# Kernel optimization log

Measured on AMD Instinct MI355X. Metric: run time of the kernel, lower is better.

The kernel has to match this reference:

```python
import jax, jax.numpy as jnp
import numpy as np

D = 768

def gru_cell(x, h, W_ih, W_hh, b_ih, b_hh):
    # torch.nn.GRUCell math
    gi = x @ W_ih.T + b_ih  # [*, 3D]
    gh = h @ W_hh.T + b_hh
    i_r, i_z, i_n = jnp.split(gi, 3, axis=-1)
    h_r, h_z, h_n = jnp.split(gh, 3, axis=-1)
    r = jax.nn.sigmoid(i_r + h_r)
    z = jax.nn.sigmoid(i_z + h_z)
    n = jnp.tanh(i_n + r * h_n)
    return (1.0 - z) * n + z * h


def setup_inputs() -> dict:
    key = jax.random.key(0)
    ks = jax.random.split(key, 16)
    S, E, N, R = 2048, 32768, 100000, 1000
    w = 0.05  # weight scale to avoid full gate saturation
    return {
        'encoder_output': jax.random.normal(ks[0], (1, D), jnp.float32),
        'sample_mask': jax.random.normal(ks[1], (S, D), jnp.float32),
        'seed_entities': jnp.arange(S, dtype=jnp.int64) if jax.config.jax_enable_x64 else jnp.arange(S, dtype=jnp.int32),
        'edge_heads': jax.random.randint(ks[2], (E,), 0, S),
        'edge_tails': jax.random.randint(ks[3], (E,), 0, N),
        'edge_type': jax.random.randint(ks[4], (E,), 0, R),
        'node2node': jnp.arange(N),
        'old_ndata': jnp.arange(N),
        'relation_embeddings': jax.random.normal(ks[5], (R, D), jnp.float32),
        'W_sub': jax.random.normal(ks[6], (D, D), jnp.float32) * w,
        'b_sub': jax.random.normal(ks[7], (D,), jnp.float32) * w,
        'W_obj': jax.random.normal(ks[8], (D, D), jnp.float32) * w,
        'b_obj': jax.random.normal(ks[9], (D,), jnp.float32) * w,
        'W_ih': jax.random.normal(ks[10], (3 * D, D), jnp.float32) * w,
        'W_hh': jax.random.normal(ks[11], (3 * D, D), jnp.float32) * w,
        'b_ih': jax.random.normal(ks[12], (3 * D,), jnp.float32) * w,
        'b_hh': jax.random.normal(ks[13], (3 * D,), jnp.float32) * w,
        'default_ndata': jax.random.normal(ks[14], (N, D), jnp.float32),  # stands in for torch.randn(768) fill
    }


def reference(encoder_output, sample_mask, seed_entities, edge_heads, edge_tails,
              edge_type, node2node, old_ndata, relation_embeddings,
              W_sub, b_sub, W_obj, b_obj, W_ih, W_hh, b_ih, b_hh, default_ndata):
    S = seed_entities.shape[0]
    E = edge_heads.shape[0]
    N = old_ndata.shape[0]

    # per-seed: sub_embedding = tanh(Linear(sample_mask[i])); r0 = GRUCell(encoder_output, sub)
    sub = jnp.tanh(sample_mask @ W_sub.T + b_sub)                    # [S, D]
    x0 = jnp.broadcast_to(encoder_output, sub.shape)                 # [S, D]
    r0 = gru_cell(x0, sub, W_ih, W_hh, b_ih, b_hh)                   # [S, D]

    # map node id -> seed position (for write-order timestamps)
    seed_pos_of_node = jnp.full((N,), -1, jnp.int32).at[seed_entities].set(
        jnp.arange(S, dtype=jnp.int32))
    edge_seed_pos = seed_pos_of_node[edge_heads]                     # [E]

    # per-edge: rj = GRUCell(r0[head], rel_emb); obj = tanh(Linear(rj))
    rel = relation_embeddings[edge_type]                             # [E, D]
    rj = gru_cell(r0[edge_heads], rel, W_ih, W_hh, b_ih, b_hh)       # [E, D]
    obj = jnp.tanh(rj @ W_obj.T + b_obj)                             # [E, D]

    # writes happen in order seed0, seed0-edges, seed1, seed1-edges, ...
    stride = jnp.int32(E + 1)
    seed_t = jnp.arange(S, dtype=jnp.int32) * stride                 # seed write times
    edge_t = edge_seed_pos * stride + 1 + jnp.arange(E, dtype=jnp.int32)

    best = jnp.full((N,), -1, jnp.int32)
    best = best.at[seed_entities].max(seed_t)
    best = best.at[edge_tails].max(edge_t)

    win_s = best[seed_entities] == seed_t
    win_e = best[edge_tails] == edge_t

    table = jnp.zeros((N, sub.shape[-1]), sub.dtype)
    table = table.at[jnp.where(win_s, seed_entities, N)].set(sub, mode='drop')
    table = table.at[jnp.where(win_e, edge_tails, N)].set(obj, mode='drop')

    ids = node2node[old_ndata]                                       # reindexed node ids
    written = best[ids] >= 0
    return jnp.where(written[:, None], table[ids], default_ndata)    # [N, D]
```

## Files before the change

kernel.cpp:

```cpp
#include <hip/hip_runtime.h>

#define D 768
#define D3 2304

typedef __bf16 bf16x8 __attribute__((ext_vector_type(8)));
typedef float f32x4 __attribute__((ext_vector_type(4)));

__device__ __forceinline__ float b2f(unsigned short u) {
    unsigned int i = ((unsigned int)u) << 16;
    return __builtin_bit_cast(float, i);
}
__device__ __forceinline__ unsigned short f2b(float f) {
    unsigned int i = __builtin_bit_cast(unsigned int, f);
    i += 0x7FFFu + ((i >> 16) & 1u);
    return (unsigned short)(i >> 16);
}
__device__ __forceinline__ float sigm(float x) { return 1.0f / (1.0f + __expf(-x)); }

typedef __attribute__((address_space(1))) const unsigned int* as1p;
typedef __attribute__((address_space(3))) unsigned int* as3p;
__device__ __forceinline__ void glds16(const unsigned short* g, unsigned short* l)
{
    __builtin_amdgcn_global_load_lds((as1p)g, (as3p)l, 16, 0, 0);
}

__global__ void k_cast(const float* __restrict__ in, unsigned short* __restrict__ out, int n)
{
    int i4 = (blockIdx.x * blockDim.x + threadIdx.x) * 4;
    if (i4 >= n) return;
    float4 v = *(const float4*)(in + i4);
    ushort4 u;
    u.x = f2b(v.x); u.y = f2b(v.y); u.z = f2b(v.z); u.w = f2b(v.w);
    *(ushort4*)(out + i4) = u;
}

template<int ACT, bool OBF>
__global__ __launch_bounds__(256)
void gemm_nt128(const unsigned short* __restrict__ A,
                const unsigned short* __restrict__ B,
                const float* __restrict__ bias,
                void* __restrict__ Cv,
                int M, const int* __restrict__ Mptr,
                int N, int K)
{
    if (Mptr) M = *Mptr;
    const int bm = blockIdx.y * 128;
    if (bm >= M) return;
    const int bn = blockIdx.x * 128;
    constexpr int BK = 32;

    __shared__ __align__(16) unsigned short As[128 * BK];
    __shared__ __align__(16) unsigned short Bs[128 * BK];

    const int tid  = threadIdx.x;
    const int wave = tid >> 6;
    const int lane = tid & 63;
    const int wr = wave >> 1, wc = wave & 1;

    const int c0 = wave * 2;
    const int sr = lane >> 2;
    const int sc = (lane & 3) << 3;

    int ra0 = bm + c0 * 16 + sr;         if (ra0 >= M) ra0 = M - 1;
    int ra1 = bm + (c0 + 1) * 16 + sr;   if (ra1 >= M) ra1 = M - 1;
    int rb0 = bn + c0 * 16 + sr;         if (rb0 >= N) rb0 = N - 1;
    int rb1 = bn + (c0 + 1) * 16 + sr;   if (rb1 >= N) rb1 = N - 1;

    const unsigned short* Ag0 = A + (size_t)ra0 * K + sc;
    const unsigned short* Ag1 = A + (size_t)ra1 * K + sc;
    const unsigned short* Bg0 = B + (size_t)rb0 * K + sc;
    const unsigned short* Bg1 = B + (size_t)rb1 * K + sc;
    unsigned short* Al0 = &As[c0 * 512];
    unsigned short* Al1 = &As[(c0 + 1) * 512];
    unsigned short* Bl0 = &Bs[c0 * 512];
    unsigned short* Bl1 = &Bs[(c0 + 1) * 512];

    const int fr = lane & 15;
    const int fk = (lane >> 4) << 3;
    const unsigned short* AsF = &As[(wr * 64 + fr) * BK + fk];
    const unsigned short* BsF = &Bs[(wc * 64 + fr) * BK + fk];

    f32x4 acc[4][4];
#pragma unroll
    for (int m = 0; m < 4; ++m)
#pragma unroll
        for (int n = 0; n < 4; ++n) acc[m][n] = (f32x4)0.0f;

    for (int k0 = 0; k0 < K; k0 += BK) {
        glds16(Ag0 + k0, Al0);
        glds16(Ag1 + k0, Al1);
        glds16(Bg0 + k0, Bl0);
        glds16(Bg1 + k0, Bl1);
        __syncthreads();
        bf16x8 a[4], b[4];
#pragma unroll
        for (int m = 0; m < 4; ++m) a[m] = *(const bf16x8*)(AsF + m * 16 * BK);
#pragma unroll
        for (int n = 0; n < 4; ++n) b[n] = *(const bf16x8*)(BsF + n * 16 * BK);
#pragma unroll
        for (int m = 0; m < 4; ++m)
#pragma unroll
            for (int n = 0; n < 4; ++n)
                acc[m][n] = __builtin_amdgcn_mfma_f32_16x16x32_bf16(a[m], b[n], acc[m][n], 0, 0, 0);
        __syncthreads();
    }

    const int rr = (lane >> 4) << 2;
    const int cc = lane & 15;
#pragma unroll
    for (int m = 0; m < 4; ++m) {
        const int row = bm + wr * 64 + m * 16 + rr;
#pragma unroll
        for (int n = 0; n < 4; ++n) {
            const int col = bn + wc * 64 + n * 16 + cc;
            if (col >= N) continue;
            const float bv = bias ? bias[col] : 0.0f;
#pragma unroll
            for (int r = 0; r < 4; ++r) {
                if (row + r < M) {
                    float v = acc[m][n][r] + bv;
                    if (ACT == 1) v = tanhf(v);
                    if (OBF) ((unsigned short*)Cv)[(size_t)(row + r) * N + col] = f2b(v);
                    else     ((float*)Cv)[(size_t)(row + r) * N + col] = v;
                }
            }
        }
    }
}

__global__ void k_gi0(const float* __restrict__ enc,
                      const float* __restrict__ Wih,
                      const float* __restrict__ bih,
                      float* __restrict__ gi0)
{
    int j = blockIdx.x * 4 + (threadIdx.x >> 6);
    int lane = threadIdx.x & 63;
    if (j >= D3) return;
    const float* w = Wih + (size_t)j * D;
    float s = 0.0f;
    for (int k = lane; k < D; k += 64) s += enc[k] * w[k];
#pragma unroll
    for (int off = 32; off > 0; off >>= 1) s += __shfl_xor(s, off, 64);
    if (lane == 0) gi0[j] = s + bih[j];
}

__global__ void k_r0(const float* __restrict__ gi0, const float* __restrict__ gh,
                     const unsigned short* __restrict__ sub,
                     unsigned short* __restrict__ r0, int S)
{
    int idx = blockIdx.x * blockDim.x + threadIdx.x;
    if (idx >= S * D) return;
    int s = idx / D, d = idx - s * D;
    const float* g = gh + (size_t)s * D3;
    float r = sigm(gi0[d] + g[d]);
    float z = sigm(gi0[D + d] + g[D + d]);
    float n = tanhf(gi0[2 * D + d] + r * g[2 * D + d]);
    float h = b2f(sub[idx]);
    r0[idx] = f2b((1.0f - z) * n + z * h);
}

__global__ void k_seed_st(const int* __restrict__ se, int* __restrict__ seed_pos,
                          int* __restrict__ best, int S, int stride)
{
    int s = blockIdx.x * blockDim.x + threadIdx.x;
    if (s >= S) return;
    int node = se[s];
    atomicMax(&seed_pos[node], s);
    atomicMax(&best[node], s * stride);
}

__global__ void k_edge_time(const int* __restrict__ heads, const int* __restrict__ tails,
                            const int* __restrict__ seed_pos, int* __restrict__ best,
                            int E, int stride)
{
    int e = blockIdx.x * blockDim.x + threadIdx.x;
    if (e >= E) return;
    int p = seed_pos[heads[e]];
    int t = p * stride + 1 + e;
    if (t < 0) return;
    atomicMax(&best[tails[e]], t);
}

__global__ void k_seed_win(const int* __restrict__ se, const int* __restrict__ best,
                           int* __restrict__ winner, int S, int stride)
{
    int s = blockIdx.x * blockDim.x + threadIdx.x;
    if (s >= S) return;
    int node = se[s];
    if (best[node] == s * stride) winner[node] = s;
}

__global__ void k_edge_win(const int* __restrict__ heads, const int* __restrict__ tails,
                           const int* __restrict__ seed_pos, const int* __restrict__ best,
                           int* __restrict__ winner, int E, int S, int stride)
{
    int e = blockIdx.x * blockDim.x + threadIdx.x;
    if (e >= E) return;
    int p = seed_pos[heads[e]];
    int t = p * stride + 1 + e;
    if (t < 0) return;
    int node = tails[e];
    if (best[node] == t) winner[node] = S + e;
}

__global__ void k_compact(const int* __restrict__ best, const int* __restrict__ winner,
                          int* __restrict__ cnt, int* __restrict__ wedge,
                          int* __restrict__ objrow, int N, int S)
{
    int n = blockIdx.x * blockDim.x + threadIdx.x;
    if (n >= N) return;
    int w = winner[n];
    if (best[n] >= 0 && w >= S) {
        int r = atomicAdd(cnt, 1);
        wedge[r] = w - S;
        objrow[n] = r;
    }
}

__global__ void k_edge2(const int* __restrict__ wedge, const int* __restrict__ cntp,
                        const int* __restrict__ heads, const int* __restrict__ types,
                        const float* __restrict__ Gi, const float* __restrict__ Ghr,
                        const float* __restrict__ rel,
                        unsigned short* __restrict__ rjw)
{
    const int W = *cntp;
    const int wave = threadIdx.x >> 6;
    const int lane = threadIdx.x & 63;
    for (int row = blockIdx.x * 4 + wave; row < W; row += gridDim.x * 4) {
        int e = wedge[row];
        int hd = heads[e], t = types[e];
        const float* gi = Gi + (size_t)hd * D3;
        const float* gh = Ghr + (size_t)t * D3;
        const float* rl = rel + (size_t)t * D;
        unsigned short* out = rjw + (size_t)row * D;
#pragma unroll
        for (int i = 0; i < 3; ++i) {
            int d = i * 256 + lane * 4;
            float4 vr = *(const float4*)(gi + d);
            float4 hr = *(const float4*)(gh + d);
            float4 vz = *(const float4*)(gi + D + d);
            float4 hz = *(const float4*)(gh + D + d);
            float4 vn = *(const float4*)(gi + 2 * D + d);
            float4 hn = *(const float4*)(gh + 2 * D + d);
            float4 hh = *(const float4*)(rl + d);
            ushort4 o;
            { float r = sigm(vr.x + hr.x), z = sigm(vz.x + hz.x);
              float n = tanhf(vn.x + r * hn.x);
              o.x = f2b((1.0f - z) * n + z * hh.x); }
            { float r = sigm(vr.y + hr.y), z = sigm(vz.y + hz.y);
              float n = tanhf(vn.y + r * hn.y);
              o.y = f2b((1.0f - z) * n + z * hh.y); }
            { float r = sigm(vr.z + hr.z), z = sigm(vz.z + hz.z);
              float n = tanhf(vn.z + r * hn.z);
              o.z = f2b((1.0f - z) * n + z * hh.z); }
            { float r = sigm(vr.w + hr.w), z = sigm(vz.w + hz.w);
              float n = tanhf(vn.w + r * hn.w);
              o.w = f2b((1.0f - z) * n + z * hh.w); }
            *(ushort4*)(out + d) = o;
        }
    }
}

__global__ void k_out(const int* __restrict__ n2n, const int* __restrict__ oldnd,
                      const int* __restrict__ best, const int* __restrict__ winner,
                      const int* __restrict__ objrow,
                      const unsigned short* __restrict__ sub,
                      const unsigned short* __restrict__ obj,
                      const float* __restrict__ defnd,
                      float* __restrict__ out, int N, int S)
{
    int idx = blockIdx.x * blockDim.x + threadIdx.x;
    const int JP = D / 4;
    if (idx >= N * JP) return;
    int i = idx / JP, j = idx - i * JP;
    int id = n2n[oldnd[i]];
    float4 v;
    if (best[id] >= 0) {
        int w = winner[id];
        const unsigned short* src = (w < S) ? sub + (size_t)w * D + j * 4
                                            : obj + (size_t)objrow[id] * D + j * 4;
        ushort4 u = *(const ushort4*)src;
        v.x = b2f(u.x); v.y = b2f(u.y); v.z = b2f(u.z); v.w = b2f(u.w);
    } else {
        v = *(const float4*)(defnd + (size_t)i * D + j * 4);
    }
    *(float4*)(out + (size_t)i * D + j * 4) = v;
}

extern "C" void kernel_launch(void* const* d_in, const int* in_sizes, int n_in,
                              void* d_out, int out_size, void* d_ws, size_t ws_size,
                              hipStream_t stream)
{
    const float* enc    = (const float*)d_in[0];
    const float* smask  = (const float*)d_in[1];
    const int* seed_ent = (const int*)d_in[2];
    const int* eheads   = (const int*)d_in[3];
    const int* etails   = (const int*)d_in[4];
    const int* etype    = (const int*)d_in[5];
    const int* n2n      = (const int*)d_in[6];
    const int* oldnd    = (const int*)d_in[7];
    const float* rel    = (const float*)d_in[8];
    const float* Wsub   = (const float*)d_in[9];
    const float* bsub   = (const float*)d_in[10];
    const float* Wobj   = (const float*)d_in[11];
    const float* bobj   = (const float*)d_in[12];
    const float* Wih    = (const float*)d_in[13];
    const float* Whh    = (const float*)d_in[14];
    const float* bih    = (const float*)d_in[15];
    const float* bhh    = (const float*)d_in[16];
    const float* defnd  = (const float*)d_in[17];

    const int S = in_sizes[2];
    const int E = in_sizes[3];
    const int N = in_sizes[6];
    const int R = in_sizes[8] / D;
    const int stride = E + 1;
    const int maxW = (E < N) ? E : N;

    char* p = (char*)d_ws;
    auto carve = [&](size_t bytes) -> char* {
        char* r = p; p += (bytes + 255) & ~(size_t)255; return r;
    };
    unsigned short* smask_b = (unsigned short*)carve((size_t)S * D * 2);
    unsigned short* Wsub_b  = (unsigned short*)carve((size_t)D * D * 2);
    unsigned short* Wobj_b  = (unsigned short*)carve((size_t)D * D * 2);
    unsigned short* Wih_b   = (unsigned short*)carve((size_t)D3 * D * 2);
    unsigned short* Whh_b   = (unsigned short*)carve((size_t)D3 * D * 2);
    unsigned short* rel_b   = (unsigned short*)carve((size_t)R * D * 2);
    unsigned short* sub     = (unsigned short*)carve((size_t)S * D * 2);
    unsigned short* r0      = (unsigned short*)carve((size_t)S * D * 2);
    unsigned short* rj      = (unsigned short*)carve((size_t)maxW * D * 2);
    unsigned short* obj     = (unsigned short*)carve((size_t)maxW * D * 2);
    float* gi0 = (float*)carve((size_t)D3 * 4);
    float* gh  = (float*)carve((size_t)S * D3 * 4);
    float* ghr = (float*)carve((size_t)R * D3 * 4);
    int* seed_pos = (int*)carve((size_t)N * 4);
    int* best     = (int*)carve((size_t)N * 4);
    int* winner   = (int*)carve((size_t)N * 4);
    int* wedge    = (int*)carve((size_t)maxW * 4);
    int* objrow   = (int*)carve((size_t)N * 4);
    int* cnt      = (int*)carve(256);

    dim3 blk(256);
    auto g1 = [](int n) { return dim3((n + 255) / 256); };
    auto gemmg = [](int M, int N_) { return dim3(N_ / 128, (M + 127) / 128); };

    hipMemsetAsync(seed_pos, 0xFF, (size_t)N * 4, stream);
    hipMemsetAsync(best,     0xFF, (size_t)N * 4, stream);
    hipMemsetAsync(winner,   0xFF, (size_t)N * 4, stream);
    hipMemsetAsync(cnt,      0x00, 4, stream);

    k_seed_st  <<<g1(S), blk, 0, stream>>>(seed_ent, seed_pos, best, S, stride);
    k_edge_time<<<g1(E), blk, 0, stream>>>(eheads, etails, seed_pos, best, E, stride);
    k_seed_win <<<g1(S), blk, 0, stream>>>(seed_ent, best, winner, S, stride);
    k_edge_win <<<g1(E), blk, 0, stream>>>(eheads, etails, seed_pos, best, winner, E, S, stride);
    k_compact  <<<g1(N), blk, 0, stream>>>(best, winner, cnt, wedge, objrow, N, S);

    k_cast<<<g1(S * D / 4),  blk, 0, stream>>>(smask, smask_b, S * D);
    k_cast<<<g1(D * D / 4),  blk, 0, stream>>>(Wsub,  Wsub_b,  D * D);
    k_cast<<<g1(D * D / 4),  blk, 0, stream>>>(Wobj,  Wobj_b,  D * D);
    k_cast<<<g1(D3 * D / 4), blk, 0, stream>>>(Wih,   Wih_b,   D3 * D);
    k_cast<<<g1(D3 * D / 4), blk, 0, stream>>>(Whh,   Whh_b,   D3 * D);
    k_cast<<<g1(R * D / 4),  blk, 0, stream>>>(rel,   rel_b,   R * D);

    gemm_nt128<1, true><<<gemmg(S, D), blk, 0, stream>>>(
        smask_b, Wsub_b, bsub, sub, S, nullptr, D, D);
    k_gi0<<<dim3((D3 + 3) / 4), blk, 0, stream>>>(enc, Wih, bih, gi0);
    gemm_nt128<0, false><<<gemmg(S, D3), blk, 0, stream>>>(
        sub, Whh_b, bhh, gh, S, nullptr, D3, D);
    k_r0<<<g1(S * D), blk, 0, stream>>>(gi0, gh, sub, r0, S);
    gemm_nt128<0, false><<<gemmg(S, D3), blk, 0, stream>>>(
        r0, Wih_b, bih, gh, S, nullptr, D3, D);
    gemm_nt128<0, false><<<gemmg(R, D3), blk, 0, stream>>>(
        rel_b, Whh_b, bhh, ghr, R, nullptr, D3, D);

    k_edge2<<<dim3(2048), blk, 0, stream>>>(wedge, cnt, eheads, etype, gh, ghr, rel, rj);
    gemm_nt128<1, true><<<gemmg(maxW, D), blk, 0, stream>>>(
        rj, Wobj_b, bobj, obj, maxW, cnt, D, D);

    k_out<<<g1(N * (D / 4)), blk, 0, stream>>>(
        n2n, oldnd, best, winner, objrow, sub, obj, defnd, (float*)d_out, N, S);
}
```

Before: 909.9 us.

## Merge casts and group winning edges by relation type via histogram scan

Six fp32-to-bf16 cast launches become one, and the four memsets become two. The seed and edge winner kernels are merged. The node-wide compaction is replaced by a per-relation-type histogram, a single-block prefix scan and a scatter, so winning edges are stored contiguously by type. The intent is fewer launches, no N-wide compaction pass, and better locality for the ghr and rel gathers in k_edge2. The cost is an extra serial scan kernel and atomics on the histogram.

```diff
diff --git a/kernel.cpp b/kernel.cpp
--- a/kernel.cpp
+++ b/kernel.cpp
@@ -24,14 +24,28 @@
     __builtin_amdgcn_global_load_lds((as1p)g, (as3p)l, 16, 0, 0);
 }
 
-__global__ void k_cast(const float* __restrict__ in, unsigned short* __restrict__ out, int n)
-{
-    int i4 = (blockIdx.x * blockDim.x + threadIdx.x) * 4;
-    if (i4 >= n) return;
-    float4 v = *(const float4*)(in + i4);
+__global__ void k_cast6(const float* __restrict__ s0, const float* __restrict__ s1,
+                        const float* __restrict__ s2, const float* __restrict__ s3,
+                        const float* __restrict__ s4, const float* __restrict__ s5,
+                        unsigned short* __restrict__ d0, unsigned short* __restrict__ d1,
+                        unsigned short* __restrict__ d2, unsigned short* __restrict__ d3,
+                        unsigned short* __restrict__ d4, unsigned short* __restrict__ d5,
+                        int c0, int c1, int c2, int c3, int c4, int c5)
+{
+    int g = blockIdx.x * blockDim.x + threadIdx.x;
+    const float* src; unsigned short* dst; int base;
+    if      (g < c0) { src = s0; dst = d0; base = 0;  }
+    else if (g < c1) { src = s1; dst = d1; base = c0; }
+    else if (g < c2) { src = s2; dst = d2; base = c1; }
+    else if (g < c3) { src = s3; dst = d3; base = c2; }
+    else if (g < c4) { src = s4; dst = d4; base = c3; }
+    else if (g < c5) { src = s5; dst = d5; base = c4; }
+    else return;
+    int i4 = (g - base) * 4;
+    float4 v = *(const float4*)(src + i4);
     ushort4 u;
     u.x = f2b(v.x); u.y = f2b(v.y); u.z = f2b(v.z); u.w = f2b(v.w);
-    *(ushort4*)(out + i4) = u;
+    *(ushort4*)(dst + i4) = u;
 }
 
 template<int ACT, bool OBF>
@@ -181,18 +195,76 @@
     atomicMax(&best[tails[e]], t);
 }
 
-__global__ void k_seed_win(const int* __restrict__ se, const int* __restrict__ best,
-                           int* __restrict__ winner, int S, int stride)
-{
-    int s = blockIdx.x * blockDim.x + threadIdx.x;
-    if (s >= S) return;
-    int node = se[s];
-    if (best[node] == s * stride) winner[node] = s;
-}
-
-__global__ void k_edge_win(const int* __restrict__ heads, const int* __restrict__ tails,
-                           const int* __restrict__ seed_pos, const int* __restrict__ best,
-                           int* __restrict__ winner, int E, int S, int stride)
+__global__ void k_win(const int* __restrict__ se,
+                      const int* __restrict__ heads, const int* __restrict__ tails,
+                      const int* __restrict__ types,
+                      const int* __restrict__ seed_pos, const int* __restrict__ best,
+                      int* __restrict__ winner, int* __restrict__ thist,
+                      int S, int E, int stride)
+{
+    int idx = blockIdx.x * blockDim.x + threadIdx.x;
+    if (idx < S) {
+        int node = se[idx];
+        if (best[node] == idx * stride) winner[node] = idx;
+    } else {
+        int e = idx - S;
+        if (e >= E) return;
+        int p = seed_pos[heads[e]];
+        int t = p * stride + 1 + e;
+        if (t < 0) return;
+        if (best[tails[e]] == t) atomicAdd(&thist[types[e]], 1);
+    }
+}
+
+__global__ void k_scan(const int* __restrict__ thist, int* __restrict__ toff,
+                       int* __restrict__ cnt, int R)
+{
+    __shared__ int wsum[4];
+    __shared__ int chunkbase;
+    const int tid  = threadIdx.x;
+    const int lane = tid & 63;
+    const int wave = tid >> 6;
+    if (tid == 0) chunkbase = 0;
+    __syncthreads();
+    for (int base0 = 0; base0 < R; base0 += 1024) {
+        int v[4]; int s = 0;
+        int base = base0 + tid * 4;
+#pragma unroll
+        for (int j = 0; j < 4; ++j) {
+            int i = base + j;
+            v[j] = (i < R) ? thist[i] : 0;
+            s += v[j];
+        }
+        int tsum = s;
+#pragma unroll
+        for (int off = 1; off < 64; off <<= 1) {
+            int o = __shfl_up(tsum, off, 64);
+            if (lane >= off) tsum += o;
+        }
+        if (lane == 63) wsum[wave] = tsum;
+        __syncthreads();
+        int wbase = 0;
+        for (int w = 0; w < 4; ++w) if (w < wave) wbase += wsum[w];
+        int run = chunkbase + wbase + (tsum - s);
+#pragma unroll
+        for (int j = 0; j < 4; ++j) {
+            int i = base + j;
+            if (i < R) toff[i] = run;
+            run += v[j];
+        }
+        __syncthreads();
+        if (tid == 0) chunkbase += wsum[0] + wsum[1] + wsum[2] + wsum[3];
+        __syncthreads();
+    }
+    if (tid == 0) *cnt = chunkbase;
+}
+
+__global__ void k_scatter(const int* __restrict__ heads, const int* __restrict__ tails,
+                          const int* __restrict__ types,
+                          const int* __restrict__ seed_pos, const int* __restrict__ best,
+                          const int* __restrict__ toff, int* __restrict__ tcur,
+                          int* __restrict__ wedge, int* __restrict__ objrow,
+                          int E, int stride)
 {
     int e = blockIdx.x * blockDim.x + threadIdx.x;
     if (e >= E) return;
@@ -200,21 +272,11 @@
     int t = p * stride + 1 + e;
     if (t < 0) return;
     int node = tails[e];
-    if (best[node] == t) winner[node] = S + e;
-}
-
-__global__ void k_compact(const int* __restrict__ best, const int* __restrict__ winner,
-                          int* __restrict__ cnt, int* __restrict__ wedge,
-                          int* __restrict__ objrow, int N, int S)
-{
-    int n = blockIdx.x * blockDim.x + threadIdx.x;
-    if (n >= N) return;
-    int w = winner[n];
-    if (best[n] >= 0 && w >= S) {
-        int r = atomicAdd(cnt, 1);
-        wedge[r] = w - S;
-        objrow[n] = r;
-    }
+    if (best[node] != t) return;
+    int ty = types[e];
+    int r = toff[ty] + atomicAdd(&tcur[ty], 1);
+    wedge[r] = e;
+    objrow[node] = r;
 }
 
 __global__ void k_edge2(const int* __restrict__ wedge, const int* __restrict__ cntp,
@@ -276,9 +338,9 @@
     int id = n2n[oldnd[i]];
     float4 v;
     if (best[id] >= 0) {
-        int w = winner[id];
-        const unsigned short* src = (w < S) ? sub + (size_t)w * D + j * 4
-                                            : obj + (size_t)objrow[id] * D + j * 4;
+        int orow = objrow[id];
+        const unsigned short* src = (orow >= 0) ? obj + (size_t)orow * D + j * 4
+                                                : sub + (size_t)winner[id] * D + j * 4;
         ushort4 u = *(const ushort4*)src;
         v.x = b2f(u.x); v.y = b2f(u.y); v.z = b2f(u.z); v.w = b2f(u.w);
     } else {
@@ -334,34 +396,42 @@
     float* gi0 = (float*)carve((size_t)D3 * 4);
     float* gh  = (float*)carve((size_t)S * D3 * 4);
     float* ghr = (float*)carve((size_t)R * D3 * 4);
-    int* seed_pos = (int*)carve((size_t)N * 4);
-    int* best     = (int*)carve((size_t)N * 4);
-    int* winner   = (int*)carve((size_t)N * 4);
-    int* wedge    = (int*)carve((size_t)maxW * 4);
-    int* objrow   = (int*)carve((size_t)N * 4);
-    int* cnt      = (int*)carve(256);
+    int* ints4    = (int*)carve((size_t)4 * N * 4);
+    int* seed_pos = ints4;
+    int* best     = ints4 + N;
+    int* winner   = ints4 + 2 * (size_t)N;
+    int* objrow   = ints4 + 3 * (size_t)N;
+    int* zblk  = (int*)carve(((size_t)3 * R + 64) * 4);
+    int* thist = zblk;
+    int* tcur  = zblk + R;
+    int* toff  = zblk + 2 * (size_t)R;
+    int* cnt   = zblk + 3 * (size_t)R;
+    int* wedge = (int*)carve((size_t)maxW * 4);
 
     dim3 blk(256);
     auto g1 = [](int n) { return dim3((n + 255) / 256); };
     auto gemmg = [](int M, int N_) { return dim3(N_ / 128, (M + 127) / 128); };
 
-    hipMemsetAsync(seed_pos, 0xFF, (size_t)N * 4, stream);
-    hipMemsetAsync(best,     0xFF, (size_t)N * 4, stream);
-    hipMemsetAsync(winner,   0xFF, (size_t)N * 4, stream);
-    hipMemsetAsync(cnt,      0x00, 4, stream);
+    hipMemsetAsync(ints4, 0xFF, (size_t)4 * N * 4, stream);
+    hipMemsetAsync(zblk,  0x00, ((size_t)3 * R + 64) * 4, stream);
+
+    const int gc0 = S * D / 4;
+    const int gc1 = gc0 + D * D / 4;
+    const int gc2 = gc1 + D * D / 4;
+    const int gc3 = gc2 + D3 * D / 4;
+    const int gc4 = gc3 + D3 * D / 4;
+    const int gc5 = gc4 + R * D / 4;
+    k_cast6<<<g1(gc5), blk, 0, stream>>>(smask, Wsub, Wobj, Wih, Whh, rel,
+                                         smask_b, Wsub_b, Wobj_b, Wih_b, Whh_b, rel_b,
+                                         gc0, gc1, gc2, gc3, gc4, gc5);
 
     k_seed_st  <<<g1(S), blk, 0, stream>>>(seed_ent, seed_pos, best, S, stride);
     k_edge_time<<<g1(E), blk, 0, stream>>>(eheads, etails, seed_pos, best, E, stride);
-    k_seed_win <<<g1(S), blk, 0, stream>>>(seed_ent, best, winner, S, stride);
-    k_edge_win <<<g1(E), blk, 0, stream>>>(eheads, etails, seed_pos, best, winner, E, S, stride);
-    k_compact  <<<g1(N), blk, 0, stream>>>(best, winner, cnt, wedge, objrow, N, S);
-
-    k_cast<<<g1(S * D / 4),  blk, 0, stream>>>(smask, smask_b, S * D);
-    k_cast<<<g1(D * D / 4),  blk, 0, stream>>>(Wsub,  Wsub_b,  D * D);
-    k_cast<<<g1(D * D / 4),  blk, 0, stream>>>(Wobj,  Wobj_b,  D * D);
-    k_cast<<<g1(D3 * D / 4), blk, 0, stream>>>(Wih,   Wih_b,   D3 * D);
-    k_cast<<<g1(D3 * D / 4), blk, 0, stream>>>(Whh,   Whh_b,   D3 * D);
-    k_cast<<<g1(R * D / 4),  blk, 0, stream>>>(rel,   rel_b,   R * D);
+    k_win      <<<g1(S + E), blk, 0, stream>>>(seed_ent, eheads, etails, etype,
+                                               seed_pos, best, winner, thist, S, E, stride);
+    k_scan     <<<dim3(1), blk, 0, stream>>>(thist, toff, cnt, R);
+    k_scatter  <<<g1(E), blk, 0, stream>>>(eheads, etails, etype, seed_pos, best,
+                                           toff, tcur, wedge, objrow, E, stride);
 
     gemm_nt128<1, true><<<gemmg(S, D), blk, 0, stream>>>(
         smask_b, Wsub_b, bsub, sub, S, nullptr, D, D);
```

Measured after the change: 867.1 us. -4.7%, faster.
